# Optimization experiments

Hardware: AMD Instinct MI355X
Metric: run time of the kernel (lower is better)

Reference implementation:

```python
import jax, jax.numpy as jnp
import numpy as np

B, H, S, D = 2, 12, 512, 64
ALL = H * D  # 768


def setup_inputs() -> dict:
    key = jax.random.key(0)
    k1, k2, k3, k4 = jax.random.split(key, 4)
    hidden_states = jax.random.normal(k1, (B, S, ALL), dtype=jnp.float32)
    # attention probs: softmax-normalized so rows sum to 1 (realistic)
    logits = jax.random.normal(k2, (B, H, S, S), dtype=jnp.float32)
    attention_probs = jax.nn.softmax(logits, axis=-1)
    value_layer = jax.random.normal(k3, (B, H, S, D), dtype=jnp.float32)
    dense_weight = jax.random.normal(k4, (ALL, ALL), dtype=jnp.float32) * 0.02
    return {"hidden_states": hidden_states, "attention_probs": attention_probs,
            "value_layer": value_layer, "dense_weight": dense_weight}


def reference(hidden_states, attention_probs, value_layer, dense_weight):
    # value_layer: [B,H,S,D]; dense_weight: [ALL,ALL] (nn.Linear weight)
    b, h, s, d = value_layer.shape
    all_head = h * d
    # [ALL,H,D] -> [H,D,ALL]: per-head slice of the output projection
    W = dense_weight.reshape(all_head, h, d).transpose(1, 2, 0)
    # transformed_layer: each head's value projected through its slice of dense
    transformed = jnp.einsum('bhsd,hde->bhse', value_layer, W)  # [B,H,S,ALL]
    transformed_norm = jnp.linalg.norm(transformed, axis=-1)    # [B,H,S]
    # ||p[b,h,k,s] * t[b,h,s,:]|| == |p| * ||t||  (exact algebraic reduction of
    # the torch code's [B,H,S,S,ALL] intermediate)
    weighted_norm = jnp.abs(attention_probs) * transformed_norm[:, :, None, :]  # [B,H,S,S]
    # sum over heads of the attention-weighted transformed values
    summed = jnp.einsum('bhks,bhse->bkse', attention_probs, transformed)  # [B,S,S,ALL]
    summed_weighted_norm = jnp.linalg.norm(summed, axis=-1)  # [B,S,S]
    return transformed_norm, weighted_norm, summed_weighted_norm, transformed
```

## Files before the change

kernel.cpp:

```cpp
#include <hip/hip_runtime.h>
#include <stdint.h>

#define B_   2
#define H_   12
#define S_   512
#define D_   64
#define ALL_ 768
#define NPAIR 78

#define OFF_TN  0
#define OFF_WN  12288
#define OFF_SWN 6303744
#define OFF_T   6828032

typedef short short4v __attribute__((ext_vector_type(4)));
typedef short short8v __attribute__((ext_vector_type(8)));
typedef float f32x4  __attribute__((ext_vector_type(4)));

__host__ __device__ constexpr int pairIdx(int h1, int h2) {
  return h1 * 12 - (h1 * (h1 - 1)) / 2 + (h2 - h1);
}

__device__ inline short f2bf(float x) {
  union { float f; uint32_t u; } c; c.f = x;
  uint32_t r = (c.u + 0x7FFFu + ((c.u >> 16) & 1u)) >> 16;
  return (short)r;
}

__global__ __launch_bounds__(256) void kernelA(const float* __restrict__ V,
                                               const float* __restrict__ W,
                                               float* __restrict__ T) {
  __shared__ char Ab[128 * 128];
  __shared__ char Bb[128 * 128];
  const int tid = threadIdx.x;
  const int et = blockIdx.x, rt = blockIdx.y, h = blockIdx.z;

#pragma unroll
  for (int p = 0; p < 8; ++p) {
    int f = tid + (p << 8);
    int row = f >> 4, c = f & 15;
    int addr = ((row << 7) + (c << 3)) ^ ((row & 7) << 4);
    int r = (rt << 7) + row;
    int b = r >> 9, s = r & 511;
    float4 v = *(const float4*)&V[((((b * H_ + h) << 9) + s) << 6) + (c << 2)];
    short4v sv = { f2bf(v.x), f2bf(v.y), f2bf(v.z), f2bf(v.w) };
    *(short4v*)(Ab + addr) = sv;
    float4 wv = *(const float4*)&W[((et << 7) + row) * ALL_ + (h << 6) + (c << 2)];
    short4v wsv = { f2bf(wv.x), f2bf(wv.y), f2bf(wv.z), f2bf(wv.w) };
    *(short4v*)(Bb + addr) = wsv;
  }
  __syncthreads();

  const int l = tid & 63, w = tid >> 6;
  const int lr = l & 15, lg = l >> 4;

  f32x4 acc[2][8];
#pragma unroll
  for (int i = 0; i < 2; ++i)
#pragma unroll
    for (int j = 0; j < 8; ++j) acc[i][j] = (f32x4){0.f, 0.f, 0.f, 0.f};

#pragma unroll
  for (int ks = 0; ks < 2; ++ks) {
    short8v a[2];
#pragma unroll
    for (int tm = 0; tm < 2; ++tm) {
      int row = (w << 5) + (tm << 4) + lr;
      int addr = ((row << 7) + (ks << 6) + (lg << 4)) ^ ((row & 7) << 4);
      a[tm] = *(short8v*)(Ab + addr);
    }
#pragma unroll
    for (int tn = 0; tn < 8; ++tn) {
      int row = (tn << 4) + lr;
      int addr = ((row << 7) + (ks << 6) + (lg << 4)) ^ ((row & 7) << 4);
      short8v bf = *(short8v*)(Bb + addr);
      acc[0][tn] = __builtin_amdgcn_mfma_f32_16x16x32_bf16(a[0], bf, acc[0][tn], 0, 0, 0);
      acc[1][tn] = __builtin_amdgcn_mfma_f32_16x16x32_bf16(a[1], bf, acc[1][tn], 0, 0, 0);
    }
  }

#pragma unroll
  for (int tm = 0; tm < 2; ++tm)
#pragma unroll
    for (int r = 0; r < 4; ++r) {
      int row = (w << 5) + (tm << 4) + (lg << 2) + r;
      int gr = (rt << 7) + row;
      int b = gr >> 9, s = gr & 511;
      float* dst = &T[(((b * H_ + h) << 9) + s) * ALL_ + (et << 7) + lr];
#pragma unroll
      for (int tn = 0; tn < 8; ++tn)
        dst[tn << 4] = acc[tm][tn][r];
    }
}

__global__ __launch_bounds__(256) void kernelB(const float* __restrict__ T,
                                               float* __restrict__ TN,
                                               float* __restrict__ GT) {
  const int tid = threadIdx.x;
  const int w = tid >> 6, lane = tid & 63;
  const int bs = (blockIdx.x << 2) + w;
  const int b = bs >> 9, s = bs & 511;

  float acc[NPAIR] = {};
#pragma unroll
  for (int j = 0; j < 3; ++j) {
    float4 tv[12];
#pragma unroll
    for (int h = 0; h < 12; ++h)
      tv[h] = *(const float4*)&T[(((b * H_ + h) << 9) + s) * ALL_ +
                                 (((j << 6) + lane) << 2)];
#pragma unroll
    for (int h1 = 0; h1 < 12; ++h1)
#pragma unroll
      for (int h2 = h1; h2 < 12; ++h2) {
        const int p = pairIdx(h1, h2);
        acc[p] = fmaf(tv[h1].x, tv[h2].x, acc[p]);
        acc[p] = fmaf(tv[h1].y, tv[h2].y, acc[p]);
        acc[p] = fmaf(tv[h1].z, tv[h2].z, acc[p]);
        acc[p] = fmaf(tv[h1].w, tv[h2].w, acc[p]);
      }
  }

#pragma unroll
  for (int p = 0; p < NPAIR; ++p) {
#pragma unroll
    for (int d = 1; d < 64; d <<= 1)
      acc[p] += __shfl_xor(acc[p], d, 64);
  }

  if (lane < 64) {
    const int p = lane;
    float v = 0.f;
#pragma unroll
    for (int q = 0; q < NPAIR; ++q)
      if (q == p) v = acc[q];
    GT[(b * NPAIR + p) * S_ + s] = v;
#pragma unroll
    for (int h = 0; h < 12; ++h)
      if (p == pairIdx(h, h)) TN[(b * H_ + h) * S_ + s] = sqrtf(v);
  }
  if (lane < NPAIR - 64) {
    const int p = 64 + lane;
    float v = 0.f;
#pragma unroll
    for (int q = 64; q < NPAIR; ++q)
      if (q == p) v = acc[q];
    GT[(b * NPAIR + p) * S_ + s] = v;
#pragma unroll
    for (int h = 0; h < 12; ++h)
      if (p == pairIdx(h, h)) TN[(b * H_ + h) * S_ + s] = sqrtf(v);
  }
}

__global__ __launch_bounds__(256) void kernelC(const float* __restrict__ P,
                                               const float* __restrict__ GT,
                                               float* __restrict__ WN,
                                               float* __restrict__ SWN) {
  const int tid = threadIdx.x;
  const int st = blockIdx.x, kt = blockIdx.y, b = blockIdx.z;
  const int sl = tid & 63, kq = tid >> 6;
  const int s = (st << 6) + sl;

  float g[NPAIR];
#pragma unroll
  for (int p = 0; p < NPAIR; ++p)
    g[p] = GT[(b * NPAIR + p) * S_ + s];
  float tn[12];
#pragma unroll
  for (int h = 0; h < 12; ++h)
    tn[h] = sqrtf(g[pairIdx(h, h)]);

#pragma unroll 1
  for (int kp = 0; kp < 4; ++kp) {
    const int k = (kt << 4) + (kp << 2) + kq;
    float pv[12];
#pragma unroll
    for (int h = 0; h < 12; ++h) {
      const int idx = (((b * H_ + h) << 9) + k) * S_ + s;
      pv[h] = P[idx];
      WN[idx] = fabsf(pv[h]) * tn[h];
    }
    float q = 0.f;
#pragma unroll
    for (int h1 = 0; h1 < 12; ++h1) {
      q = fmaf(pv[h1] * pv[h1], g[pairIdx(h1, h1)], q);
#pragma unroll
      for (int h2 = h1 + 1; h2 < 12; ++h2)
        q = fmaf(2.f * pv[h1] * pv[h2], g[pairIdx(h1, h2)], q);
    }
    SWN[((b << 9) + k) * S_ + s] = sqrtf(fmaxf(q, 0.f));
  }
}

extern "C" void kernel_launch(void* const* d_in, const int* in_sizes, int n_in,
                              void* d_out, int out_size, void* d_ws, size_t ws_size,
                              hipStream_t stream) {
  const float* P = (const float*)d_in[1];
  const float* V = (const float*)d_in[2];
  const float* W = (const float*)d_in[3];
  float* out = (float*)d_out;
  float* GT = (float*)d_ws;

  kernelA<<<dim3(6, 8, 12), 256, 0, stream>>>(V, W, out + OFF_T);
  kernelB<<<dim3(256), 256, 0, stream>>>(out + OFF_T, out + OFF_TN, GT);
  kernelC<<<dim3(8, 32, 2), 256, 0, stream>>>(P, GT, out + OFF_WN, out + OFF_SWN);
}
```

Baseline: 42.69 us.

## Compute head Gram matrix with bf16 MFMA and shrink kernelA tiles

kernelB used to compute the 78 per-position head-pair dot products with scalar FMAs and then reduce each one across the wavefront with shuffles. It now builds the 12x12 Gram matrix per position with 16x16x32 bf16 MFMA, feeding the same operand as both A and B, which removes the large register array and the shuffle reductions. kernelA is retiled to 64-row blocks of 128 threads, doubling the grid, to get more blocks in flight. The cost is bf16 rounding of T inside the Gram computation, which lowers the accuracy of the norms, and 4 of the 16 lanes in each group sit idle.

```diff
diff --git a/kernel.cpp b/kernel.cpp
--- a/kernel.cpp
+++ b/kernel.cpp
@@ -27,24 +27,30 @@
   return (short)r;
 }
 
-__global__ __launch_bounds__(256) void kernelA(const float* __restrict__ V,
+__global__ __launch_bounds__(128) void kernelA(const float* __restrict__ V,
                                                const float* __restrict__ W,
                                                float* __restrict__ T) {
-  __shared__ char Ab[128 * 128];
+  __shared__ char Ab[64 * 128];
   __shared__ char Bb[128 * 128];
   const int tid = threadIdx.x;
   const int et = blockIdx.x, rt = blockIdx.y, h = blockIdx.z;
 
 #pragma unroll
   for (int p = 0; p < 8; ++p) {
-    int f = tid + (p << 8);
+    int f = tid + (p << 7);
     int row = f >> 4, c = f & 15;
     int addr = ((row << 7) + (c << 3)) ^ ((row & 7) << 4);
-    int r = (rt << 7) + row;
+    int r = (rt << 6) + row;
     int b = r >> 9, s = r & 511;
     float4 v = *(const float4*)&V[((((b * H_ + h) << 9) + s) << 6) + (c << 2)];
     short4v sv = { f2bf(v.x), f2bf(v.y), f2bf(v.z), f2bf(v.w) };
     *(short4v*)(Ab + addr) = sv;
+  }
+#pragma unroll
+  for (int p = 0; p < 16; ++p) {
+    int f = tid + (p << 7);
+    int row = f >> 4, c = f & 15;
+    int addr = ((row << 7) + (c << 3)) ^ ((row & 7) << 4);
     float4 wv = *(const float4*)&W[((et << 7) + row) * ALL_ + (h << 6) + (c << 2)];
     short4v wsv = { f2bf(wv.x), f2bf(wv.y), f2bf(wv.z), f2bf(wv.w) };
     *(short4v*)(Bb + addr) = wsv;
@@ -84,7 +90,7 @@
 #pragma unroll
     for (int r = 0; r < 4; ++r) {
       int row = (w << 5) + (tm << 4) + (lg << 2) + r;
-      int gr = (rt << 7) + row;
+      int gr = (rt << 6) + row;
       int b = gr >> 9, s = gr & 511;
       float* dst = &T[(((b * H_ + h) << 9) + s) * ALL_ + (et << 7) + lr];
 #pragma unroll
@@ -97,58 +103,37 @@
                                                float* __restrict__ TN,
                                                float* __restrict__ GT) {
   const int tid = threadIdx.x;
-  const int w = tid >> 6, lane = tid & 63;
+  const int w = tid >> 6, l = tid & 63;
   const int bs = (blockIdx.x << 2) + w;
   const int b = bs >> 9, s = bs & 511;
+  const int col = l & 15, lg = l >> 4;
 
-  float acc[NPAIR] = {};
+  const float* rowp = T + (((b * H_ + col) << 9) + s) * ALL_;
+  const bool act = col < 12;
+
+  f32x4 acc = (f32x4){0.f, 0.f, 0.f, 0.f};
 #pragma unroll
-  for (int j = 0; j < 3; ++j) {
-    float4 tv[12];
-#pragma unroll
-    for (int h = 0; h < 12; ++h)
-      tv[h] = *(const float4*)&T[(((b * H_ + h) << 9) + s) * ALL_ +
-                                 (((j << 6) + lane) << 2)];
-#pragma unroll
-    for (int h1 = 0; h1 < 12; ++h1)
-#pragma unroll
-      for (int h2 = h1; h2 < 12; ++h2) {
-        const int p = pairIdx(h1, h2);
-        acc[p] = fmaf(tv[h1].x, tv[h2].x, acc[p]);
-        acc[p] = fmaf(tv[h1].y, tv[h2].y, acc[p]);
-        acc[p] = fmaf(tv[h1].z, tv[h2].z, acc[p]);
-        acc[p] = fmaf(tv[h1].w, tv[h2].w, acc[p]);
-      }
+  for (int kk = 0; kk < 24; ++kk) {
+    const int e = (kk << 5) + (lg << 3);
+    short8v x = (short8v){0, 0, 0, 0, 0, 0, 0, 0};
+    if (act) {
+      float4 u0 = *(const float4*)(rowp + e);
+      float4 u1 = *(const float4*)(rowp + e + 4);
+      x = (short8v){f2bf(u0.x), f2bf(u0.y), f2bf(u0.z), f2bf(u0.w),
+                    f2bf(u1.x), f2bf(u1.y), f2bf(u1.z), f2bf(u1.w)};
+    }
+    acc = __builtin_amdgcn_mfma_f32_16x16x32_bf16(x, x, acc, 0, 0, 0);
   }
 
 #pragma unroll
-  for (int p = 0; p < NPAIR; ++p) {
-#pragma unroll
-    for (int d = 1; d < 64; d <<= 1)
-      acc[p] += __shfl_xor(acc[p], d, 64);
-  }
-
-  if (lane < 64) {
-    const int p = lane;
-    float v = 0.f;
-#pragma unroll
-    for (int q = 0; q < NPAIR; ++q)
-      if (q == p) v = acc[q];
-    GT[(b * NPAIR + p) * S_ + s] = v;
-#pragma unroll
-    for (int h = 0; h < 12; ++h)
-      if (p == pairIdx(h, h)) TN[(b * H_ + h) * S_ + s] = sqrtf(v);
-  }
-  if (lane < NPAIR - 64) {
-    const int p = 64 + lane;
-    float v = 0.f;
-#pragma unroll
-    for (int q = 64; q < NPAIR; ++q)
-      if (q == p) v = acc[q];
-    GT[(b * NPAIR + p) * S_ + s] = v;
-#pragma unroll
-    for (int h = 0; h < 12; ++h)
-      if (p == pairIdx(h, h)) TN[(b * H_ + h) * S_ + s] = sqrtf(v);
+  for (int r = 0; r < 4; ++r) {
+    const int rw = (lg << 2) + r;
+    const float v = acc[r];
+    if (col < 12 && rw <= col) {
+      const int p = rw * 12 - (rw * (rw - 1)) / 2 + (col - rw);
+      GT[(b * NPAIR + p) * S_ + s] = v;
+      if (rw == col) TN[(b * H_ + col) * S_ + s] = sqrtf(v);
+    }
   }
 }
 
@@ -201,7 +186,7 @@
   float* out = (float*)d_out;
   float* GT = (float*)d_ws;
 
-  kernelA<<<dim3(6, 8, 12), 256, 0, stream>>>(V, W, out + OFF_T);
+  kernelA<<<dim3(6, 16, 12), 128, 0, stream>>>(V, W, out + OFF_T);
   kernelB<<<dim3(256), 256, 0, stream>>>(out + OFF_T, out + OFF_TN, GT);
   kernelC<<<dim3(8, 32, 2), 256, 0, stream>>>(P, GT, out + OFF_WN, out + OFF_SWN);
 }
```

Measured after the change: 40.23 us. 5.8% less time.
